# Optimization experiments

Hardware: AMD Instinct MI355X
Metric: run time of the kernel (lower is better)

Reference implementation:

```python
import jax, jax.numpy as jnp
from jax import lax
import numpy as np

INPUT_SIZE = 3
RESERVOIR = 2048
OUTPUT_SIZE = 3
SPECTRAL_RADIUS = 0.9
SPARSITY = 0.1
B, T = 16, 2048


def setup_inputs() -> dict:
    key = jax.random.key(0)
    kx, kwin, kw, kmask, kwo, kb = jax.random.split(key, 6)
    x = jax.random.normal(kx, (B, T, INPUT_SIZE), dtype=jnp.float32)
    Win = jax.random.normal(kwin, (RESERVOIR, INPUT_SIZE), dtype=jnp.float32)
    W = jax.random.normal(kw, (RESERVOIR, RESERVOIR), dtype=jnp.float32)
    # spectral-radius rescale (circular law: rho(randn(R,R)) ~ sqrt(R)), then sparsify
    W = W * (SPECTRAL_RADIUS / jnp.sqrt(jnp.float32(RESERVOIR)))
    mask = (jax.random.uniform(kmask, (RESERVOIR, RESERVOIR)) < SPARSITY).astype(jnp.float32)
    W = W * mask
    bound = 1.0 / np.sqrt(RESERVOIR)
    Wout_w = jax.random.uniform(kwo, (OUTPUT_SIZE, RESERVOIR), minval=-bound, maxval=bound, dtype=jnp.float32)
    Wout_b = jax.random.uniform(kb, (OUTPUT_SIZE,), minval=-bound, maxval=bound, dtype=jnp.float32)
    return {"x": x, "Win": Win, "W": W, "Wout_w": Wout_w, "Wout_b": Wout_b}


def reference(x, Win, W, Wout_w, Wout_b):
    Bsz = x.shape[0]
    R = W.shape[0]
    h0 = jnp.zeros((Bsz, R), dtype=x.dtype)

    def step(h, xt):
        h_new = jnp.tanh(xt @ Win.T + h @ W.T)  # [B, R]
        return h_new, h_new

    _, hs = lax.scan(step, h0, jnp.swapaxes(x, 0, 1))  # hs: [T, B, R]
    outs = hs @ Wout_w.T + Wout_b  # [T, B, O]
    return jnp.swapaxes(outs, 0, 1)  # [B, T, O]
```

## Files before the change

### kernel.cpp

```cpp
#include <hip/hip_runtime.h>
#include <math.h>


#define RDIM   2048
#define BATCH  16
#define TSTEPS 2048
#define NIN    3
#define NOUT   3
#define NBLK   256
#define NTHR   512

typedef unsigned u32x2 __attribute__((ext_vector_type(2)));

#define HT0_DW     0
#define HT1_DW     16384
#define WS_USED_DW 32768

#define POLL_MAX   (1L << 14)

__device__ __forceinline__ void st1_uc(unsigned* p, unsigned v) {
    asm volatile("global_store_dword %0, %1, off sc0 sc1" :: "v"(p), "v"(v) : "memory");
}

__device__ __forceinline__ int q8(float v) {
    float c = fminf(127.f, fmaxf(-127.f, v));
    return (int)__builtin_rintf(c);
}
__device__ __forceinline__ unsigned pack4(int a, int b, int c, int d) {
    return (a & 0xff) | ((b & 0xff) << 8) | ((c & 0xff) << 16) | ((d & 0xff) << 24);
}
__device__ __forceinline__ int dot4i(unsigned a, unsigned b, int c) {
#if __has_builtin(__builtin_amdgcn_sdot4)
    return __builtin_amdgcn_sdot4((int)a, (int)b, c, false);
#else
    c += (int)(signed char)(a) * (int)(signed char)(b);
    c += (int)(signed char)(a >> 8)  * (int)(signed char)(b >> 8);
    c += (int)(signed char)(a >> 16) * (int)(signed char)(b >> 16);
    c += (int)(signed char)(a >> 24) * (int)(signed char)(b >> 24);
    return c;
#endif
}
__device__ __forceinline__ int dot16(uint4 wq, uint4 hq, int c) {
    c = dot4i(wq.x, hq.x, c);
    c = dot4i(wq.y, hq.y, c);
    c = dot4i(wq.z, hq.z, c);
    c = dot4i(wq.w, hq.w, c);
    return c;
}

extern "C" __global__ void __launch_bounds__(NTHR, 1) esn_persist(
    const float* __restrict__ W,
    const float* __restrict__ Win,
    const float* __restrict__ x,
    const float* __restrict__ Wout,
    const float* __restrict__ bout,
    unsigned* wsu,
    float* __restrict__ out)
{
    __shared__ int red[2][8][8][17];
    __shared__ __align__(16) unsigned hstage[2][2][512];
    __shared__ float wscale[64];
    extern __shared__ unsigned wlds[];

    const int tid  = threadIdx.x;
    const int lane = tid & 63;
    const int w    = tid >> 6;
    const int blk  = blockIdx.x;
    const int rg   = blk & 31;
    const int g    = blk >> 5;
    const int b0    = g * 2;
    const int kslot = lane >> 3;
    const int rgrp  = lane & 7;

#pragma unroll
    for (int rr = 0; rr < 8; ++rr) {
        const int   row = rg * 64 + w * 8 + rr;
        const float4* Wr = (const float4*)(W + (size_t)row * RDIM);
        float m = 0.f;
#pragma unroll
        for (int j = 0; j < 8; ++j) {
            float4 v = Wr[j * 64 + lane];
            m = fmaxf(m, fmaxf(fmaxf(fabsf(v.x), fabsf(v.y)),
                               fmaxf(fabsf(v.z), fabsf(v.w))));
        }
#pragma unroll
        for (int off = 32; off >= 1; off >>= 1)
            m = fmaxf(m, __shfl_xor(m, off, 64));
        const float inv = (m > 0.f) ? 127.f / m : 0.f;
        if (lane == 0) wscale[w * 8 + rr] = (m > 0.f) ? m / 127.f : 0.f;
#pragma unroll
        for (int j = 0; j < 8; ++j) {
            float4 v = Wr[j * 64 + lane];
            const int gsw = (j * 16 + (lane >> 2)) ^ w;
            wlds[(w * 8 + rr) * 512 + gsw * 4 + (lane & 3)] =
                pack4(q8(v.x * inv), q8(v.y * inv), q8(v.z * inv), q8(v.w * inv));
        }
    }

    float wn0 = 0.f, wn1 = 0.f, wn2 = 0.f;
    if (tid < 128) {
        const float* wp = Win + (size_t)(rg * 64 + (tid >> 1)) * NIN;
        wn0 = wp[0]; wn1 = wp[1]; wn2 = wp[2];
    }
    __syncthreads();

    unsigned* const ht0 = wsu + HT0_DW;
    unsigned* const ht1 = wsu + HT1_DW;

    u32x2 ta, tb;
    {
        const unsigned* pA0 = ht0 + g * 2048 +        128 * w + 2 * lane;
        const unsigned* pB0 = ht0 + g * 2048 + 1024 + 128 * w + 2 * lane;
        asm volatile("global_load_dwordx2 %0, %2, off sc0 sc1\n\t"
                     "global_load_dwordx2 %1, %3, off sc0 sc1"
                     : "=&v"(ta), "=&v"(tb) : "v"(pA0), "v"(pB0) : "memory");
    }
    int dly = 6;

    for (int t = 0; t <= TSTEPS; ++t) {
        unsigned* const hb  = (t & 1) ? ht1 : ht0;
        unsigned* const hbn = (t & 1) ? ht0 : ht1;
        const unsigned tg  = (unsigned)t & 0xffffu;
        const unsigned tg1 = (unsigned)(t + 1) & 0xffffu;
        const int par = t & 1;

        bool first_hit;
        {
            const unsigned* pA = hb + g * 2048 +        128 * w + 2 * lane;
            const unsigned* pB = hb + g * 2048 + 1024 + 128 * w + 2 * lane;
            asm volatile("s_waitcnt vmcnt(0)" : "+v"(ta), "+v"(tb) :: "memory");
            bool ok = (ta[0] >> 16) == tg && (ta[1] >> 16) == tg &&
                      (tb[0] >> 16) == tg && (tb[1] >> 16) == tg;
            first_hit = ok;
            long r = 0;
            while (!ok && r <= POLL_MAX) {
                ++r;
                if (r > 1) __builtin_amdgcn_s_sleep(2);
                asm volatile("global_load_dwordx2 %0, %2, off sc0 sc1\n\t"
                             "global_load_dwordx2 %1, %3, off sc0 sc1\n\t"
                             "s_waitcnt vmcnt(0)"
                             : "=&v"(ta), "=&v"(tb) : "v"(pA), "v"(pB) : "memory");
                ok = (ta[0] >> 16) == tg && (ta[1] >> 16) == tg &&
                     (tb[0] >> 16) == tg && (tb[1] >> 16) == tg;
            }
        }
        dly += __all((int)first_hit) ? -1 : 4;
        dly = dly < 0 ? 0 : (dly > 24 ? 24 : dly);

        const unsigned pdA = (ta[0] & 0xffffu) | (ta[1] << 16);
        const unsigned pdB = (tb[0] & 0xffffu) | (tb[1] << 16);
        hstage[par][0][(w << 6) + lane] = pdA;
        hstage[par][1][(w << 6) + lane] = pdB;

        float xv0 = 0.f, xv1 = 0.f, xv2 = 0.f;
        if (t < TSTEPS && tid < 128) {
            const float* xp = x + ((size_t)(b0 + (tid & 1)) * TSTEPS + t) * NIN;
            xv0 = xp[0]; xv1 = xp[1]; xv2 = xp[2];
        }

        if (t < TSTEPS) {
            const uint4* hwA = (const uint4*)&hstage[par][0][(w << 6) + (kslot << 3)];
            const uint4* hwB = (const uint4*)&hstage[par][1][(w << 6) + (kslot << 3)];
            const uint4 hA0 = hwA[0], hA1 = hwA[1];
            const uint4 hB0 = hwB[0], hB1 = hwB[1];

            int acc[8][2];
#pragma unroll
            for (int rr = 0; rr < 8; ++rr) { acc[rr][0] = 0; acc[rr][1] = 0; }
            const uint4* w4p = (const uint4*)wlds;
            const int g0 = (w << 4) + (((kslot << 1) ^ rgrp) & 15);
#pragma unroll
            for (int rr = 0; rr < 8; ++rr) {
                const int gi = (((rgrp << 3) + rr) << 7);
                uint4 w0 = w4p[gi + g0];
                uint4 w1 = w4p[gi + (g0 ^ 1)];
                acc[rr][0] = dot16(w0, hA0, acc[rr][0]);
                acc[rr][0] = dot16(w1, hA1, acc[rr][0]);
                acc[rr][1] = dot16(w0, hB0, acc[rr][1]);
                acc[rr][1] = dot16(w1, hB1, acc[rr][1]);
            }
#pragma unroll
            for (int rr = 0; rr < 8; ++rr)
#pragma unroll
                for (int b = 0; b < 2; ++b) {
                    int a = acc[rr][b];
                    a += __shfl_xor(a, 8, 64);
                    a += __shfl_xor(a, 16, 64);
                    a += __shfl_xor(a, 32, 64);
                    acc[rr][b] = a;
                }
            if (lane < 8) {
#pragma unroll
                for (int rr = 0; rr < 8; ++rr) {
                    red[par][w][lane][(rr << 1)]     = acc[rr][0];
                    red[par][w][lane][(rr << 1) + 1] = acc[rr][1];
                }
            }
        }
        __syncthreads();

        if (t < TSTEPS && tid < 128) {
            const int br = tid >> 1;
            const int b  = tid & 1;
            int s = 0;
#pragma unroll
            for (int wp = 0; wp < 8; ++wp)
                s += red[par][wp][br >> 3][((br & 7) << 1) + b];
            float pre = (float)s * wscale[br] * (1.f / 127.f)
                      + wn0 * xv0 + wn1 * xv1 + wn2 * xv2;
            const int qv = q8(tanhf(pre) * 127.f);
            const int qlo = __shfl(qv, ((lane >> 1) << 2) + (lane & 1), 64);
            const int qhi = __shfl(qv, ((lane >> 1) << 2) + 2 + (lane & 1), 64);
            if (lane < 32) {
                const int bb = lane & 1;
                const int u  = (w << 4) + (lane >> 1);
                unsigned dv = (unsigned)(qlo & 0xff) |
                              ((unsigned)(qhi & 0xff) << 8) | (tg1 << 16);
                st1_uc(hbn + g * 2048 + bb * 1024 + rg * 32 + u, dv);
            }
        }

        if (t > 0 && rg == ((t - 1) & 31) && w >= 2) {
            const int pw = w - 2;
            const int b  = pw / NOUT;
            const int k  = pw % NOUT;
            const float4* wo4 = (const float4*)(Wout + (size_t)k * RDIM);
            float a = 0.f;
#pragma unroll
            for (int j = 0; j < 8; ++j) {
                unsigned hv = hstage[par][b][(lane << 3) + j];
                float4 wf = wo4[(lane << 3) + j];
                a += (float)(int)(signed char)(hv & 0xff)         * wf.x;
                a += (float)(int)(signed char)((hv >> 8) & 0xff)  * wf.y;
                a += (float)(int)(signed char)((hv >> 16) & 0xff) * wf.z;
                a += (float)(int)(signed char)(hv >> 24)          * wf.w;
            }
#pragma unroll
            for (int off = 32; off >= 1; off >>= 1)
                a += __shfl_xor(a, off, 64);
            if (lane == 0)
                out[((size_t)(b0 + b) * TSTEPS + (t - 1)) * NOUT + k] =
                    a * (1.f / 127.f) + bout[k];
        }

        if (t < TSTEPS) {
            for (int i = 0; i < dly; ++i) __builtin_amdgcn_s_sleep(1);
            const unsigned* nA = hbn + g * 2048 +        128 * w + 2 * lane;
            const unsigned* nB = hbn + g * 2048 + 1024 + 128 * w + 2 * lane;
            asm volatile("global_load_dwordx2 %0, %2, off sc0 sc1\n\t"
                         "global_load_dwordx2 %1, %3, off sc0 sc1"
                         : "=&v"(ta), "=&v"(tb) : "v"(nA), "v"(nB) : "memory");
        }
    }
}

extern "C" void kernel_launch(void* const* d_in, const int* in_sizes, int n_in,
                              void* d_out, int out_size, void* d_ws, size_t ws_size,
                              hipStream_t stream) {
    const float* x    = (const float*)d_in[0];
    const float* Win  = (const float*)d_in[1];
    const float* W    = (const float*)d_in[2];
    const float* Wout = (const float*)d_in[3];
    const float* bout = (const float*)d_in[4];
    float* out = (float*)d_out;
    unsigned* wsu = (unsigned*)d_ws;

    hipMemsetAsync(d_ws, 0, (size_t)WS_USED_DW * sizeof(unsigned), stream);

    hipFuncSetAttribute((const void*)esn_persist,
                        hipFuncAttributeMaxDynamicSharedMemorySize, 131072);

    void* args[] = {(void*)&W, (void*)&Win, (void*)&x, (void*)&Wout, (void*)&bout,
                    (void*)&wsu, (void*)&out};
    hipError_t e = hipLaunchCooperativeKernel((const void*)esn_persist,
                                              dim3(NBLK), dim3(NTHR),
                                              args, 131072, stream);
    if (e != hipSuccess) {
        esn_persist<<<dim3(NBLK), dim3(NTHR), 131072, stream>>>(
            W, Win, x, Wout, bout, wsu, out);
    }
}
```

Measured before the change: 6.280 ms.

## Issue early speculative flag prefetch, move delayed load before output, use fast tanh

Each step now issues two loads of the next hidden-state buffer: an early speculative one right after the barrier, and the usual delayed one, which is moved ahead of the output projection. The waiter checks the early copy first using a partial vmcnt wait and falls back to the later copy or polling when the tags are stale. This aims to shorten the cross-block handoff latency in the persistent recurrence. tanhf is also replaced with an exp/rcp approximation, which may slightly change quantized outputs, and the vmcnt counting depends on which waves issued output-path loads, which is fragile.

```diff
diff --git a/kernel.cpp b/kernel.cpp
--- a/kernel.cpp
+++ b/kernel.cpp
@@ -18,13 +18,26 @@
 
 #define POLL_MAX   (1L << 14)
 
+#define TAGOK(a, b, t) (((a)[0] >> 16) == (t) && ((a)[1] >> 16) == (t) && \
+                        ((b)[0] >> 16) == (t) && ((b)[1] >> 16) == (t))
+
 __device__ __forceinline__ void st1_uc(unsigned* p, unsigned v) {
     asm volatile("global_store_dword %0, %1, off sc0 sc1" :: "v"(p), "v"(v) : "memory");
+}
+__device__ __forceinline__ void pf_issue(u32x2& a, u32x2& b,
+                                         const unsigned* pA, const unsigned* pB) {
+    asm volatile("global_load_dwordx2 %0, %2, off sc0 sc1\n\t"
+                 "global_load_dwordx2 %1, %3, off sc0 sc1"
+                 : "+v"(a), "+v"(b) : "v"(pA), "v"(pB) : "memory");
 }
 
 __device__ __forceinline__ int q8(float v) {
     float c = fminf(127.f, fmaxf(-127.f, v));
     return (int)__builtin_rintf(c);
+}
+__device__ __forceinline__ float fast_tanh(float x) {
+    float e2 = __expf(2.f * x);
+    return 1.f - 2.f * __builtin_amdgcn_rcpf(e2 + 1.f);
 }
 __device__ __forceinline__ unsigned pack4(int a, int b, int c, int d) {
     return (a & 0xff) | ((b & 0xff) << 8) | ((c & 0xff) << 16) | ((d & 0xff) << 24);
@@ -107,13 +120,12 @@
     unsigned* const ht0 = wsu + HT0_DW;
     unsigned* const ht1 = wsu + HT1_DW;
 
-    u32x2 ta, tb;
+    u32x2 ta = {0, 0}, tb = {0, 0}, tae = {0, 0}, tbe = {0, 0};
     {
         const unsigned* pA0 = ht0 + g * 2048 +        128 * w + 2 * lane;
         const unsigned* pB0 = ht0 + g * 2048 + 1024 + 128 * w + 2 * lane;
-        asm volatile("global_load_dwordx2 %0, %2, off sc0 sc1\n\t"
-                     "global_load_dwordx2 %1, %3, off sc0 sc1"
-                     : "=&v"(ta), "=&v"(tb) : "v"(pA0), "v"(pB0) : "memory");
+        pf_issue(tae, tbe, pA0, pB0);
+        pf_issue(ta,  tb,  pA0, pB0);
     }
     int dly = 6;
 
@@ -128,9 +140,16 @@
         {
             const unsigned* pA = hb + g * 2048 +        128 * w + 2 * lane;
             const unsigned* pB = hb + g * 2048 + 1024 + 128 * w + 2 * lane;
-            asm volatile("s_waitcnt vmcnt(0)" : "+v"(ta), "+v"(tb) :: "memory");
-            bool ok = (ta[0] >> 16) == tg && (ta[1] >> 16) == tg &&
-                      (tb[0] >> 16) == tg && (tb[1] >> 16) == tg;
+            if (w < 2 && t > 0)
+                asm volatile("s_waitcnt vmcnt(3)" : "+v"(tae), "+v"(tbe) :: "memory");
+            else
+                asm volatile("s_waitcnt vmcnt(2)" : "+v"(tae), "+v"(tbe) :: "memory");
+            bool ok = TAGOK(tae, tbe, tg);
+            if (ok) { ta = tae; tb = tbe; }
+            if (!ok) {
+                asm volatile("s_waitcnt vmcnt(0)" : "+v"(ta), "+v"(tb) :: "memory");
+                ok = TAGOK(ta, tb, tg);
+            }
             first_hit = ok;
             long r = 0;
             while (!ok && r <= POLL_MAX) {
@@ -139,9 +158,8 @@
                 asm volatile("global_load_dwordx2 %0, %2, off sc0 sc1\n\t"
                              "global_load_dwordx2 %1, %3, off sc0 sc1\n\t"
                              "s_waitcnt vmcnt(0)"
-                             : "=&v"(ta), "=&v"(tb) : "v"(pA), "v"(pB) : "memory");
-                ok = (ta[0] >> 16) == tg && (ta[1] >> 16) == tg &&
-                     (tb[0] >> 16) == tg && (tb[1] >> 16) == tg;
+                             : "+v"(ta), "+v"(tb) : "v"(pA), "v"(pB) : "memory");
+                ok = TAGOK(ta, tb, tg);
             }
         }
         dly += __all((int)first_hit) ? -1 : 4;
@@ -199,6 +217,14 @@
         }
         __syncthreads();
 
+        if (t < TSTEPS) {
+            asm volatile("s_waitcnt vmcnt(0)"
+                         : "+v"(ta), "+v"(tb), "+v"(tae), "+v"(tbe) :: "memory");
+            const unsigned* nA = hbn + g * 2048 +        128 * w + 2 * lane;
+            const unsigned* nB = hbn + g * 2048 + 1024 + 128 * w + 2 * lane;
+            pf_issue(tae, tbe, nA, nB);
+        }
+
         if (t < TSTEPS && tid < 128) {
             const int br = tid >> 1;
             const int b  = tid & 1;
@@ -208,7 +234,7 @@
                 s += red[par][wp][br >> 3][((br & 7) << 1) + b];
             float pre = (float)s * wscale[br] * (1.f / 127.f)
                       + wn0 * xv0 + wn1 * xv1 + wn2 * xv2;
-            const int qv = q8(tanhf(pre) * 127.f);
+            const int qv = q8(fast_tanh(pre) * 127.f);
             const int qlo = __shfl(qv, ((lane >> 1) << 2) + (lane & 1), 64);
             const int qhi = __shfl(qv, ((lane >> 1) << 2) + 2 + (lane & 1), 64);
             if (lane < 32) {
@@ -220,6 +246,13 @@
             }
         }
 
+        if (t < TSTEPS) {
+            for (int i = 0; i < dly; ++i) __builtin_amdgcn_s_sleep(1);
+            const unsigned* nA = hbn + g * 2048 +        128 * w + 2 * lane;
+            const unsigned* nB = hbn + g * 2048 + 1024 + 128 * w + 2 * lane;
+            pf_issue(ta, tb, nA, nB);
+        }
+
         if (t > 0 && rg == ((t - 1) & 31) && w >= 2) {
             const int pw = w - 2;
             const int b  = pw / NOUT;
@@ -241,15 +274,6 @@
             if (lane == 0)
                 out[((size_t)(b0 + b) * TSTEPS + (t - 1)) * NOUT + k] =
                     a * (1.f / 127.f) + bout[k];
-        }
-
-        if (t < TSTEPS) {
-            for (int i = 0; i < dly; ++i) __builtin_amdgcn_s_sleep(1);
-            const unsigned* nA = hbn + g * 2048 +        128 * w + 2 * lane;
-            const unsigned* nB = hbn + g * 2048 + 1024 + 128 * w + 2 * lane;
-            asm volatile("global_load_dwordx2 %0, %2, off sc0 sc1\n\t"
-                         "global_load_dwordx2 %1, %3, off sc0 sc1"
-                         : "=&v"(ta), "=&v"(tb) : "v"(nA), "v"(nB) : "memory");
         }
     }
 }
```

Result: slower. 6.481 ms (+3.2%).

## Interleave h exchange buffer for single dwordx4 poll and prefetch x earlier

Applied to the files above, without the earlier changes.

Reorders the global hidden-state exchange layout so each lane's two batch halves sit contiguously, letting one dwordx4 load replace two dwordx2 loads for both the prefetch and the spin-poll. The next step's x is loaded one iteration ahead, and the prefetch of the next h buffer is issued before the output projection instead of after it. This cuts memory instructions per poll and moves the poll earlier, at the cost of a different store address pattern for producers and the output projection now overlapping the in-flight load.

```diff
diff --git a/kernel.cpp b/kernel.cpp
--- a/kernel.cpp
+++ b/kernel.cpp
@@ -10,7 +10,7 @@
 #define NBLK   256
 #define NTHR   512
 
-typedef unsigned u32x2 __attribute__((ext_vector_type(2)));
+typedef unsigned u32x4 __attribute__((ext_vector_type(4)));
 
 #define HT0_DW     0
 #define HT1_DW     16384
@@ -18,8 +18,15 @@
 
 #define POLL_MAX   (1L << 14)
 
+#define TAGOK4(v, t) (((v)[0] >> 16) == (t) && ((v)[1] >> 16) == (t) && \
+                      ((v)[2] >> 16) == (t) && ((v)[3] >> 16) == (t))
+
 __device__ __forceinline__ void st1_uc(unsigned* p, unsigned v) {
     asm volatile("global_store_dword %0, %1, off sc0 sc1" :: "v"(p), "v"(v) : "memory");
+}
+__device__ __forceinline__ void pf_issue4(u32x4& v, const unsigned* p) {
+    asm volatile("global_load_dwordx4 %0, %1, off sc0 sc1"
+                 : "+v"(v) : "v"(p) : "memory");
 }
 
 __device__ __forceinline__ int q8(float v) {
@@ -107,13 +114,14 @@
     unsigned* const ht0 = wsu + HT0_DW;
     unsigned* const ht1 = wsu + HT1_DW;
 
-    u32x2 ta, tb;
-    {
-        const unsigned* pA0 = ht0 + g * 2048 +        128 * w + 2 * lane;
-        const unsigned* pB0 = ht0 + g * 2048 + 1024 + 128 * w + 2 * lane;
-        asm volatile("global_load_dwordx2 %0, %2, off sc0 sc1\n\t"
-                     "global_load_dwordx2 %1, %3, off sc0 sc1"
-                     : "=&v"(ta), "=&v"(tb) : "v"(pA0), "v"(pB0) : "memory");
+    const int woff = ((w << 6) + lane) << 2;
+
+    u32x4 tv = {0, 0, 0, 0};
+    pf_issue4(tv, ht0 + g * 2048 + woff);
+    float xv0 = 0.f, xv1 = 0.f, xv2 = 0.f;
+    if (tid < 128) {
+        const float* xp = x + ((size_t)(b0 + (tid & 1)) * TSTEPS + 0) * NIN;
+        xv0 = xp[0]; xv1 = xp[1]; xv2 = xp[2];
     }
     int dly = 6;
 
@@ -126,37 +134,27 @@
 
         bool first_hit;
         {
-            const unsigned* pA = hb + g * 2048 +        128 * w + 2 * lane;
-            const unsigned* pB = hb + g * 2048 + 1024 + 128 * w + 2 * lane;
-            asm volatile("s_waitcnt vmcnt(0)" : "+v"(ta), "+v"(tb) :: "memory");
-            bool ok = (ta[0] >> 16) == tg && (ta[1] >> 16) == tg &&
-                      (tb[0] >> 16) == tg && (tb[1] >> 16) == tg;
+            const unsigned* p = hb + g * 2048 + woff;
+            asm volatile("s_waitcnt vmcnt(0)" : "+v"(tv) :: "memory");
+            bool ok = TAGOK4(tv, tg);
             first_hit = ok;
             long r = 0;
             while (!ok && r <= POLL_MAX) {
                 ++r;
                 if (r > 1) __builtin_amdgcn_s_sleep(2);
-                asm volatile("global_load_dwordx2 %0, %2, off sc0 sc1\n\t"
-                             "global_load_dwordx2 %1, %3, off sc0 sc1\n\t"
+                asm volatile("global_load_dwordx4 %0, %1, off sc0 sc1\n\t"
                              "s_waitcnt vmcnt(0)"
-                             : "=&v"(ta), "=&v"(tb) : "v"(pA), "v"(pB) : "memory");
-                ok = (ta[0] >> 16) == tg && (ta[1] >> 16) == tg &&
-                     (tb[0] >> 16) == tg && (tb[1] >> 16) == tg;
+                             : "+v"(tv) : "v"(p) : "memory");
+                ok = TAGOK4(tv, tg);
             }
         }
         dly += __all((int)first_hit) ? -1 : 4;
         dly = dly < 0 ? 0 : (dly > 24 ? 24 : dly);
 
-        const unsigned pdA = (ta[0] & 0xffffu) | (ta[1] << 16);
-        const unsigned pdB = (tb[0] & 0xffffu) | (tb[1] << 16);
+        const unsigned pdA = (tv[0] & 0xffffu) | (tv[1] << 16);
+        const unsigned pdB = (tv[2] & 0xffffu) | (tv[3] << 16);
         hstage[par][0][(w << 6) + lane] = pdA;
         hstage[par][1][(w << 6) + lane] = pdB;
-
-        float xv0 = 0.f, xv1 = 0.f, xv2 = 0.f;
-        if (t < TSTEPS && tid < 128) {
-            const float* xp = x + ((size_t)(b0 + (tid & 1)) * TSTEPS + t) * NIN;
-            xv0 = xp[0]; xv1 = xp[1]; xv2 = xp[2];
-        }
 
         if (t < TSTEPS) {
             const uint4* hwA = (const uint4*)&hstage[par][0][(w << 6) + (kslot << 3)];
@@ -216,8 +214,19 @@
                 const int u  = (w << 4) + (lane >> 1);
                 unsigned dv = (unsigned)(qlo & 0xff) |
                               ((unsigned)(qhi & 0xff) << 8) | (tg1 << 16);
-                st1_uc(hbn + g * 2048 + bb * 1024 + rg * 32 + u, dv);
-            }
+                st1_uc(hbn + g * 2048 + 64 * rg + ((u >> 1) << 2)
+                           + (u & 1) + (bb << 1), dv);
+            }
+        }
+
+        if (t + 1 < TSTEPS && tid < 128) {
+            const float* xp = x + ((size_t)(b0 + (tid & 1)) * TSTEPS + (t + 1)) * NIN;
+            xv0 = xp[0]; xv1 = xp[1]; xv2 = xp[2];
+        }
+
+        if (t < TSTEPS) {
+            for (int i = 0; i < dly; ++i) __builtin_amdgcn_s_sleep(1);
+            pf_issue4(tv, hbn + g * 2048 + woff);
         }
 
         if (t > 0 && rg == ((t - 1) & 31) && w >= 2) {
@@ -241,15 +250,6 @@
             if (lane == 0)
                 out[((size_t)(b0 + b) * TSTEPS + (t - 1)) * NOUT + k] =
                     a * (1.f / 127.f) + bout[k];
-        }
-
-        if (t < TSTEPS) {
-            for (int i = 0; i < dly; ++i) __builtin_amdgcn_s_sleep(1);
-            const unsigned* nA = hbn + g * 2048 +        128 * w + 2 * lane;
-            const unsigned* nB = hbn + g * 2048 + 1024 + 128 * w + 2 * lane;
-            asm volatile("global_load_dwordx2 %0, %2, off sc0 sc1\n\t"
-                         "global_load_dwordx2 %1, %3, off sc0 sc1"
-                         : "=&v"(ta), "=&v"(tb) : "v"(nA), "v"(nB) : "memory");
         }
     }
 }
```

After: 6.114 ms. -2.7%, faster.
